# Kernel tuning notes

Hardware: AMD Instinct MI355X
Metric: run time of the kernel (lower is better)

## Reference

```python
import jax, jax.numpy as jnp
import numpy as np

SEQ, PREV, BS, D_IN, H, D = 512, 512, 8, 1024, 16, 64


def setup_inputs() -> dict:
    key = jax.random.key(0)
    ks = jax.random.split(key, 10)
    s = 0.02
    inp = {
        "input_": jax.random.normal(ks[0], (SEQ, BS, D_IN), jnp.float32),
        "pos_embs": jax.random.normal(ks[1], (SEQ + PREV, D_IN), jnp.float32),
        "memory": jax.random.normal(ks[2], (PREV, BS, D_IN), jnp.float32),
        "u": jax.random.normal(ks[3], (H, D), jnp.float32) * s,
        "v": jax.random.normal(ks[4], (H, D), jnp.float32) * s,
        # causal mask allowing full attention to memory: triu with diagonal=1+prev
        "mask": (jnp.triu(jnp.ones((SEQ, SEQ + PREV), jnp.bool_), k=1 + PREV))[..., None],
        "W_kv": jax.random.normal(ks[5], (D_IN, 2 * H * D), jnp.float32) * s,
        "W_q": jax.random.normal(ks[6], (D_IN, H * D), jnp.float32) * s,
        "W_p": jax.random.normal(ks[7], (D_IN, H * D), jnp.float32) * s,
        "W_out": jax.random.normal(ks[8], (H * D, D_IN), jnp.float32) * s,
        "ln_gamma": jnp.ones((D_IN,), jnp.float32),
        "ln_beta": jnp.zeros((D_IN,), jnp.float32),
    }
    return inp


def _rel_shift(x):
    # x: (q, k, bs, H) -> pad one zero column, reshape-transpose trick, drop first row
    q, k, bs, h = x.shape
    zp = jnp.zeros((q, 1, bs, h), x.dtype)
    return jnp.concatenate([zp, x], axis=1).reshape(k + 1, q, bs, h)[1:].reshape(q, k, bs, h)


def reference(input_, pos_embs, memory, u, v, mask, W_kv, W_q, W_p, W_out, ln_gamma, ln_beta):
    cur_seq, bs, d_in = input_.shape
    prev_seq = memory.shape[0]
    tot = cur_seq + prev_seq
    h, d = u.shape
    scale = 1.0 / d ** 0.5

    iwm = jnp.concatenate([memory, input_], axis=0)          # (tot, bs, d_in)
    kv = jnp.einsum('jbe,ef->jbf', iwm, W_kv)                 # (tot, bs, 2*H*d)
    k_t, v_t = jnp.split(kv, 2, axis=-1)
    q_t = jnp.einsum('ibe,ef->ibf', input_, W_q)              # (cur, bs, H*d)

    q4 = q_t.reshape(cur_seq, bs, h, d)
    k4 = k_t.reshape(tot, bs, h, d)
    v4 = v_t.reshape(tot, bs, h, d)

    content_attn = jnp.einsum('ibhd,jbhd->ijbh', q4 + u, k4)  # (cur, tot, bs, H)

    p_t = (pos_embs @ W_p).reshape(tot, h, d)                 # (tot, H, d)
    position_attn = jnp.einsum('ibhd,jhd->ijbh', q4 + v, p_t)
    position_attn = _rel_shift(position_attn)

    attn = content_attn + position_attn
    attn = jnp.where(mask[..., None], -jnp.inf, attn)         # mask: (cur, tot, 1) -> (cur, tot, 1, 1)
    attn = jax.nn.softmax(attn * scale, axis=1)

    awv = jnp.einsum('ijbh,jbhd->ibhd', attn, v4).reshape(cur_seq, bs, h * d)
    out = input_ + awv @ W_out                                # residual

    mu = jnp.mean(out, axis=-1, keepdims=True)
    var = jnp.mean((out - mu) ** 2, axis=-1, keepdims=True)
    out = (out - mu) / jnp.sqrt(var + 1e-5) * ln_gamma + ln_beta
    return out
```

## Files before the change

### kernel.cpp

```cpp
#include <hip/hip_runtime.h>
#include <math.h>

#define SEQ  512
#define PREV 512
#define TOT  1024
#define BSZ  8
#define DIN  1024
#define NH   16
#define HD   64

typedef __bf16 bf16;
typedef __bf16 bf16x8 __attribute__((ext_vector_type(8)));
typedef float  f32x4  __attribute__((ext_vector_type(4)));
typedef float  f32x16 __attribute__((ext_vector_type(16)));
typedef unsigned int u32;
typedef u32 u32x2 __attribute__((ext_vector_type(2)));

__device__ __forceinline__ f32x4 MFMA16(bf16x8 a, bf16x8 b, f32x4 c) {
    return __builtin_amdgcn_mfma_f32_16x16x32_bf16(a, b, c, 0, 0, 0);
}
__device__ __forceinline__ f32x16 MFMA32(bf16x8 a, bf16x8 b, f32x16 c) {
    return __builtin_amdgcn_mfma_f32_32x32x16_bf16(a, b, c, 0, 0, 0);
}

#define GLOAD16(g, l) __builtin_amdgcn_global_load_lds( \
    (const __attribute__((address_space(1))) void*)(g), \
    (__attribute__((address_space(3))) void*)(l), 16, 0, 0)

__device__ __forceinline__ unsigned short bfbits(float x) {
    return __builtin_bit_cast(unsigned short, (bf16)x);
}
__device__ __forceinline__ float bf2f(u32 bits16) {
    return __builtin_bit_cast(float, bits16 << 16);
}

__global__ __launch_bounds__(256) void cast_cat(
    const float* __restrict__ A, int nA, const float* __restrict__ B,
    bf16* __restrict__ out)
{
    int e4 = (blockIdx.x * 256 + threadIdx.x) * 4;
    float4 x = (e4 < nA) ? *(const float4*)(A + e4) : *(const float4*)(B + e4 - nA);
    union { bf16 h[4]; ushort4 u4; } pk;
    pk.h[0] = (bf16)x.x; pk.h[1] = (bf16)x.y; pk.h[2] = (bf16)x.z; pk.h[3] = (bf16)x.w;
    *(ushort4*)(out + e4) = pk.u4;
}

__global__ __launch_bounds__(256) void transcast_all(
    const float* __restrict__ W_kv, const float* __restrict__ W_q,
    const float* __restrict__ W_p,  const float* __restrict__ W_out,
    bf16* __restrict__ wkv, bf16* __restrict__ wq,
    bf16* __restrict__ wp,  bf16* __restrict__ wo)
{
    __shared__ float tile[32][33];
    const int bx = blockIdx.x;
    const float* W; bf16* Wt; int N, bn;
    if (bx < 64)       { W = W_kv;  Wt = wkv; N = 2048; bn = bx * 32; }
    else if (bx < 96)  { W = W_q;   Wt = wq;  N = 1024; bn = (bx - 64) * 32; }
    else if (bx < 128) { W = W_p;   Wt = wp;  N = 1024; bn = (bx - 96) * 32; }
    else               { W = W_out; Wt = wo;  N = 1024; bn = (bx - 128) * 32; }
    const int t = threadIdx.x;
    const int bk = blockIdx.y * 32;
    const int r = t >> 3, c4 = (t & 7) * 4;
    float4 x = *(const float4*)(W + (size_t)(bk + r) * N + bn + c4);
    tile[r][c4 + 0] = x.x; tile[r][c4 + 1] = x.y;
    tile[r][c4 + 2] = x.z; tile[r][c4 + 3] = x.w;
    __syncthreads();
    union { bf16 h[4]; ushort4 u4; } pk;
#pragma unroll
    for (int i = 0; i < 4; ++i) pk.h[i] = (bf16)tile[c4 + i][r];
    *(ushort4*)(Wt + (size_t)(bn + r) * 1024 + bk + c4) = pk.u4;
}

template<int FOUT>
__global__ __launch_bounds__(256) void gemm_mfma(
    const bf16* __restrict__ A, const bf16* __restrict__ Bt,
    const float* __restrict__ Rres, bf16* __restrict__ Cb,
    float* __restrict__ Cf, int M, int N, int K)
{
    __shared__ __align__(16) bf16 A_s[128 * 64];
    __shared__ __align__(16) bf16 B_s[128 * 64];
    const int t = threadIdx.x;
    const int w = t >> 6, lane = t & 63;
    const int li = lane & 15, hi = lane >> 4;
    const int wr = w >> 1, wc = w & 1;
    const int bm = blockIdx.y * 128, bn = blockIdx.x * 128;
    const int l3 = lane >> 3, l7 = lane & 7;
    const int srcoct = ((l7 ^ l3) * 8);

    f32x4 acc[4][4];
#pragma unroll
    for (int m = 0; m < 4; ++m)
#pragma unroll
        for (int n = 0; n < 4; ++n) acc[m][n] = (f32x4){0.f, 0.f, 0.f, 0.f};

    auto stage = [&](int k0) {
#pragma unroll
        for (int i = 0; i < 4; ++i) {
            int c = w * 4 + i;
            const bf16* ga = A + (size_t)(bm + c * 8 + l3) * K + k0 + srcoct;
            GLOAD16(ga, &A_s[c * 512]);
            const bf16* gb = Bt + (size_t)(bn + c * 8 + l3) * K + k0 + srcoct;
            GLOAD16(gb, &B_s[c * 512]);
        }
    };

    stage(0);
    const int nk = K >> 6;
    for (int ks = 0; ks < nk; ++ks) {
        __syncthreads();
#pragma unroll
        for (int kk = 0; kk < 2; ++kk) {
            bf16x8 af[4], bfr[4];
#pragma unroll
            for (int m = 0; m < 4; ++m) {
                int row = wr * 64 + m * 16 + li;
                af[m] = *(const bf16x8*)&A_s[row * 64 + ((kk * 32 + hi * 8) ^ ((row & 7) * 8))];
            }
#pragma unroll
            for (int n = 0; n < 4; ++n) {
                int row = wc * 64 + n * 16 + li;
                bfr[n] = *(const bf16x8*)&B_s[row * 64 + ((kk * 32 + hi * 8) ^ ((row & 7) * 8))];
            }
#pragma unroll
            for (int m = 0; m < 4; ++m)
#pragma unroll
                for (int n = 0; n < 4; ++n)
                    acc[m][n] = MFMA16(af[m], bfr[n], acc[m][n]);
        }
        __syncthreads();
        if (ks + 1 < nk) stage((ks + 1) << 6);
    }

#pragma unroll
    for (int m = 0; m < 4; ++m)
#pragma unroll
        for (int n = 0; n < 4; ++n)
#pragma unroll
            for (int r = 0; r < 4; ++r) {
                int row = bm + wr * 64 + m * 16 + hi * 4 + r;
                int col = bn + wc * 64 + n * 16 + li;
                size_t off = (size_t)row * N + col;
                if (FOUT) Cf[off] = acc[m][n][r] + Rres[off];
                else      Cb[off] = (bf16)acc[m][n][r];
            }
}

__global__ __launch_bounds__(256, 2) void attn_mfma(
    const bf16* __restrict__ kv, const bf16* __restrict__ qb,
    const bf16* __restrict__ pb, const float* __restrict__ u,
    const float* __restrict__ v, bf16* __restrict__ awv)
{
    const int bi = (blockIdx.z & 1) ? (3 - blockIdx.x) : blockIdx.x;
    const int i0 = bi * 128;
    const int b  = blockIdx.y;
    const int h  = blockIdx.z;
    const int t  = threadIdx.x;
    const int w  = t >> 6;
    const int lane = t & 63;
    const int ql  = lane & 31;
    const int hi2 = lane >> 5;

    __shared__ __align__(16) bf16 K_s[64 * 64];
    __shared__ __align__(16) bf16 V_s[64][72];
    __shared__ __align__(16) bf16 P_s[256 * 64];
    __shared__ __align__(16) char SCR[4][6912];

    char* rsc = SCR[w];
    char* ps  = SCR[w];

    const int c8 = t & 7;
    const int rq = t >> 3;
    const int nt = 2 * bi + 10;
    const int C0 = 384 - i0;

    bf16x8 vreg[2];
#pragma unroll
    for (int p = 0; p < 2; ++p)
        vreg[p] = *(const bf16x8*)(kv + (size_t)((p * 32 + rq) * BSZ + b) * 2048 + 1024 + h * HD + c8 * 8);
#pragma unroll
    for (int p = 0; p < 2; ++p)
        GLOAD16(kv + (size_t)((p * 32 + rq) * BSZ + b) * 2048 + h * HD + ((c8 ^ (rq & 7)) * 8),
                K_s + (p * 32 + rq) * 64 + c8 * 8);
#pragma unroll
    for (int cp = 0; cp < 6; ++cp) {
        int grow = C0 + cp * 32 + rq;
        GLOAD16(pb + (size_t)grow * DIN + h * HD + ((c8 ^ (rq & 7)) * 8),
                P_s + (grow & 255) * 64 + c8 * 8);
    }

    bf16x8 qu[4], qv[4];
    {
        const size_t qoff = ((size_t)(i0 + w * 32 + ql) * BSZ + b) * DIN + h * HD;
#pragma unroll
        for (int kk = 0; kk < 4; ++kk) {
            bf16x8 q8 = *(const bf16x8*)(qb + qoff + kk * 16 + hi2 * 8);
            const float* up = u + h * HD + kk * 16 + hi2 * 8;
            const float* vp = v + h * HD + kk * 16 + hi2 * 8;
#pragma unroll
            for (int m = 0; m < 8; ++m) {
                float qf = (float)q8[m];
                qu[kk][m] = (bf16)(qf + up[m]);
                qv[kk][m] = (bf16)(qf + vp[m]);
            }
        }
    }

    float mrun = -1e30f, lrun = 0.f;
    f32x16 o[2];
    o[0] = (f32x16){}; o[1] = (f32x16){};

    const int phq = (31 - ql) & 3;
    const int sel = phq >> 1;
    const int shb = (phq & 1) * 16;

    for (int tt = 0; tt < nt; ++tt) {
        const int j0 = tt * 64;

        __builtin_amdgcn_s_barrier();
        __builtin_amdgcn_sched_barrier(0);

#pragma unroll
        for (int p = 0; p < 2; ++p) {
            int j = p * 32 + rq;
#pragma unroll
            for (int mm = 0; mm < 8; ++mm)
                V_s[c8 * 8 + mm][(j + 8 * c8) & 63] = vreg[p][mm];
        }
        asm volatile("s_waitcnt vmcnt(0) lgkmcnt(0)" ::: "memory");
        __builtin_amdgcn_sched_barrier(0);
        __builtin_amdgcn_s_barrier();
        __builtin_amdgcn_sched_barrier(0);

        f32x16 st[2];
        st[0] = (f32x16){}; st[1] = (f32x16){};
        __builtin_amdgcn_s_setprio(1);
#pragma unroll
        for (int jt = 0; jt < 2; ++jt) {
            int row = jt * 32 + ql;
#pragma unroll
            for (int kk = 0; kk < 4; ++kk) {
                bf16x8 kf = *(const bf16x8*)&K_s[row * 64 + (((kk * 2 + hi2) ^ (ql & 7)) * 8)];
                st[jt] = MFMA32(kf, qu[kk], st[jt]);
            }
        }
        const int bwg = j0 - i0 + 480 - 32 * w;
        f32x16 rp[3];
        rp[0] = (f32x16){}; rp[1] = (f32x16){}; rp[2] = (f32x16){};
#pragma unroll
        for (int Rt = 0; Rt < 3; ++Rt) {
            int ring = (bwg + Rt * 32 + ql) & 255;
#pragma unroll
            for (int kk = 0; kk < 4; ++kk) {
                bf16x8 pf = *(const bf16x8*)&P_s[ring * 64 + (((kk * 2 + hi2) ^ (ring & 7)) * 8)];
                rp[Rt] = MFMA32(pf, qv[kk], rp[Rt]);
            }
        }
        __builtin_amdgcn_s_setprio(0);

        __builtin_amdgcn_s_barrier();
        __builtin_amdgcn_sched_barrier(0);

        if (tt + 1 < nt) {
            const int j0n = j0 + 64;
#pragma unroll
            for (int p = 0; p < 2; ++p)
                vreg[p] = *(const bf16x8*)(kv + (size_t)((j0n + p * 32 + rq) * BSZ + b) * 2048 + 1024 + h * HD + c8 * 8);
#pragma unroll
            for (int p = 0; p < 2; ++p)
                GLOAD16(kv + (size_t)((j0n + p * 32 + rq) * BSZ + b) * 2048 + h * HD + ((c8 ^ (rq & 7)) * 8),
                        K_s + (p * 32 + rq) * 64 + c8 * 8);
        }
        if (tt + 3 < nt) {
            const int Cs = C0 + (tt + 3) * 64;
#pragma unroll
            for (int p = 0; p < 2; ++p) {
                int grow = Cs + p * 32 + rq;
                GLOAD16(pb + (size_t)grow * DIN + h * HD + ((c8 ^ (rq & 7)) * 8),
                        P_s + (grow & 255) * 64 + c8 * 8);
            }
        }

#pragma unroll
        for (int Rt = 0; Rt < 3; ++Rt)
#pragma unroll
            for (int a = 0; a < 4; ++a) {
                u32 lo = (u32)bfbits(rp[Rt][a * 4 + 0]) | ((u32)bfbits(rp[Rt][a * 4 + 1]) << 16);
                u32 hi = (u32)bfbits(rp[Rt][a * 4 + 2]) | ((u32)bfbits(rp[Rt][a * 4 + 3]) << 16);
                *(u32x2*)(rsc + ql * 216 + 64 * Rt + 16 * a + 8 * hi2) = (u32x2){lo, hi};
            }

        float rowmax = -1e30f;
        const int limb = i0 + 32 * w + ql + PREV - j0;
#pragma unroll
        for (int jt = 0; jt < 2; ++jt)
#pragma unroll
            for (int a = 0; a < 4; ++a) {
                int e = jt * 32 + 8 * a + 4 * hi2 + 31 - ql;
                const u32x2* W = (const u32x2*)(rsc + ql * 216 + 8 * (e >> 2));
                u32x2 A0 = W[0], A1 = W[1];
                u32 U0 = sel ? A0[1] : A0[0];
                u32 U1 = sel ? A1[0] : A0[1];
                u32 U2 = sel ? A1[1] : A1[0];
                u32 o0 = (u32)((((unsigned long long)U1 << 32) | U0) >> shb);
                u32 o1 = (u32)((((unsigned long long)U2 << 32) | U1) >> shb);
                float pv0 = bf2f(o0 & 0xffffu), pv1 = bf2f(o0 >> 16);
                float pv2 = bf2f(o1 & 0xffffu), pv3 = bf2f(o1 >> 16);
                float pq[4] = {pv0, pv1, pv2, pv3};
#pragma unroll
                for (int rr = 0; rr < 4; ++rr) {
                    int r = a * 4 + rr;
                    int lj = jt * 32 + 8 * a + 4 * hi2 + rr;
                    float sv = (st[jt][r] + pq[rr]) * 0.125f;
                    if (lj > limb) sv = -1e30f;
                    st[jt][r] = sv;
                    rowmax = fmaxf(rowmax, sv);
                }
            }
        rowmax = fmaxf(rowmax, __shfl_xor(rowmax, 32));

        if (!__all(rowmax - mrun <= 8.f)) {
            float newm = fmaxf(mrun, rowmax);
            float fsc = __expf(mrun - newm);
#pragma unroll
            for (int r = 0; r < 16; ++r) {
                float fr = __shfl(fsc, (r & 3) + 8 * (r >> 2) + 4 * hi2);
                o[0][r] *= fr; o[1][r] *= fr;
            }
            lrun *= fsc;
            mrun = newm;
        }
        float rowsum = 0.f;
#pragma unroll
        for (int jt = 0; jt < 2; ++jt)
#pragma unroll
            for (int r = 0; r < 16; ++r) {
                float p = __expf(st[jt][r] - mrun);
                st[jt][r] = p;
                rowsum += p;
            }
        rowsum += __shfl_xor(rowsum, 32);
        lrun += rowsum;

#pragma unroll
        for (int jt = 0; jt < 2; ++jt)
#pragma unroll
            for (int a = 0; a < 4; ++a) {
                u32 lo = (u32)bfbits(st[jt][a * 4 + 0]) | ((u32)bfbits(st[jt][a * 4 + 1]) << 16);
                u32 hi = (u32)bfbits(st[jt][a * 4 + 2]) | ((u32)bfbits(st[jt][a * 4 + 3]) << 16);
                *(u32x2*)(ps + ql * 144 + 64 * jt + 16 * a + 8 * hi2) = (u32x2){lo, hi};
            }

        __builtin_amdgcn_s_setprio(1);
#pragma unroll
        for (int js = 0; js < 4; ++js) {
            bf16x8 pa = *(const bf16x8*)(ps + ql * 144 + 32 * js + 16 * hi2);
#pragma unroll
            for (int dt = 0; dt < 2; ++dt) {
                int dcol = dt * 32 + ql;
                int colb = (js * 16 + hi2 * 8 + 8 * (dcol >> 3)) & 63;
                bf16x8 vf = *(const bf16x8*)&V_s[dcol][colb];
                o[dt] = MFMA32(pa, vf, o[dt]);
            }
        }
        __builtin_amdgcn_s_setprio(0);
    }

    float lr[16];
#pragma unroll
    for (int r = 0; r < 16; ++r) lr[r] = __shfl(lrun, (r & 3) + 8 * (r >> 2) + 4 * hi2);
#pragma unroll
    for (int dt = 0; dt < 2; ++dt)
#pragma unroll
        for (int r = 0; r < 16; ++r) {
            int row = i0 + 32 * w + (r & 3) + 8 * (r >> 2) + 4 * hi2;
            awv[((size_t)row * BSZ + b) * DIN + h * HD + dt * 32 + ql] = (bf16)(o[dt][r] / lr[r]);
        }
}

__global__ __launch_bounds__(256) void ln_f32(
    float* __restrict__ out, const float* __restrict__ gamma, const float* __restrict__ beta)
{
    const int row = blockIdx.x;
    const int t = threadIdx.x;
    float4 x = *(float4*)(out + (size_t)row * DIN + t * 4);
    float s  = x.x + x.y + x.z + x.w;
    float ss = x.x * x.x + x.y * x.y + x.z * x.z + x.w * x.w;
#pragma unroll
    for (int wd = 1; wd < 64; wd <<= 1) { s += __shfl_xor(s, wd); ss += __shfl_xor(ss, wd); }
    __shared__ float sbuf[4], ssbuf[4];
    const int wave = t >> 6, lanei = t & 63;
    if (lanei == 0) { sbuf[wave] = s; ssbuf[wave] = ss; }
    __syncthreads();
    s  = sbuf[0] + sbuf[1] + sbuf[2] + sbuf[3];
    ss = ssbuf[0] + ssbuf[1] + ssbuf[2] + ssbuf[3];
    const float mu   = s * (1.f / DIN);
    const float var  = ss * (1.f / DIN) - mu * mu;
    const float rstd = rsqrtf(var + 1e-5f);
    float4 g  = *(const float4*)(gamma + t * 4);
    float4 bb = *(const float4*)(beta + t * 4);
    float4 y;
    y.x = (x.x - mu) * rstd * g.x + bb.x;
    y.y = (x.y - mu) * rstd * g.y + bb.y;
    y.z = (x.z - mu) * rstd * g.z + bb.z;
    y.w = (x.w - mu) * rstd * g.w + bb.w;
    *(float4*)(out + (size_t)row * DIN + t * 4) = y;
}

extern "C" void kernel_launch(void* const* d_in, const int* in_sizes, int n_in,
                              void* d_out, int out_size, void* d_ws, size_t ws_size,
                              hipStream_t stream)
{
    const float* input_ = (const float*)d_in[0];
    const float* pos    = (const float*)d_in[1];
    const float* memory = (const float*)d_in[2];
    const float* u      = (const float*)d_in[3];
    const float* v      = (const float*)d_in[4];
    const float* W_kv   = (const float*)d_in[6];
    const float* W_q    = (const float*)d_in[7];
    const float* W_p    = (const float*)d_in[8];
    const float* W_out  = (const float*)d_in[9];
    const float* gamma  = (const float*)d_in[10];
    const float* beta   = (const float*)d_in[11];

    bf16* iwm  = (bf16*)d_ws;
    bf16* kvb  = iwm  + (size_t)8192 * 1024;
    bf16* qbf  = kvb  + (size_t)8192 * 2048;
    bf16* pbf  = qbf  + (size_t)4096 * 1024;
    bf16* posb = pbf  + (size_t)1024 * 1024;
    bf16* wkv  = posb + (size_t)1024 * 1024;
    bf16* wq   = wkv  + (size_t)2048 * 1024;
    bf16* wp   = wq   + (size_t)1024 * 1024;
    bf16* wo   = wp   + (size_t)1024 * 1024;
    bf16* awvb = wo   + (size_t)1024 * 1024;
    float* outf = (float*)d_out;

    cast_cat<<<8192, 256, 0, stream>>>(memory, 4194304, input_, iwm);
    cast_cat<<<1024, 256, 0, stream>>>(pos, 1048576, pos, posb);
    transcast_all<<<dim3(160, 32), 256, 0, stream>>>(W_kv, W_q, W_p, W_out, wkv, wq, wp, wo);

    gemm_mfma<0><<<dim3(16, 64), 256, 0, stream>>>(iwm, wkv, nullptr, kvb, nullptr, 8192, 2048, 1024);
    gemm_mfma<0><<<dim3(8, 32), 256, 0, stream>>>(iwm + (size_t)4096 * 1024, wq, nullptr, qbf, nullptr, 4096, 1024, 1024);
    gemm_mfma<0><<<dim3(8, 8),  256, 0, stream>>>(posb, wp, nullptr, pbf, nullptr, 1024, 1024, 1024);

    attn_mfma<<<dim3(4, 8, 16), 256, 0, stream>>>(kvb, qbf, pbf, u, v, awvb);

    gemm_mfma<1><<<dim3(8, 32), 256, 0, stream>>>(awvb, wo, input_, nullptr, outf, 4096, 1024, 1024);
    ln_f32<<<4096, 256, 0, stream>>>(outf, gamma, beta);
}
```

Measured before the change: 205.3 us.

## Add 256x256 phased GEMM for KV projection, fuse cast kernels, use exp2 softmax

Replaces the KV projection GEMM with a new 512-thread kernel that uses 256x256 tiles and double-buffered LDS. It splits each K-step into four phases, interleaving staging loads and MFMA batches with explicit waitcnt and barriers, and remaps blocks so each XCD gets a group of neighbouring M tiles. The two cast kernels become one launch. The attention softmax folds log2(e) into the scale and uses exp2, with the rescale threshold raised to match. The aim is more data reuse and overlap in the largest GEMM and less launch and exp overhead, at the cost of one block per CU and high register pressure.

```diff
diff --git a/kernel.cpp b/kernel.cpp
--- a/kernel.cpp
+++ b/kernel.cpp
@@ -34,15 +34,24 @@
     return __builtin_bit_cast(float, bits16 << 16);
 }
 
-__global__ __launch_bounds__(256) void cast_cat(
-    const float* __restrict__ A, int nA, const float* __restrict__ B,
-    bf16* __restrict__ out)
-{
-    int e4 = (blockIdx.x * 256 + threadIdx.x) * 4;
-    float4 x = (e4 < nA) ? *(const float4*)(A + e4) : *(const float4*)(B + e4 - nA);
+__global__ __launch_bounds__(256) void cast_all(
+    const float* __restrict__ memory, const float* __restrict__ input_,
+    const float* __restrict__ pos, bf16* __restrict__ iwm, bf16* __restrict__ posb)
+{
+    const int bid = blockIdx.x;
+    const float* src; bf16* dst; int e4;
+    if (bid < 8192) {
+        e4 = (bid * 256 + threadIdx.x) * 4;
+        src = (e4 < 4194304) ? memory : input_ - 4194304;
+        dst = iwm;
+    } else {
+        e4 = ((bid - 8192) * 256 + threadIdx.x) * 4;
+        src = pos; dst = posb;
+    }
+    float4 x = *(const float4*)(src + e4);
     union { bf16 h[4]; ushort4 u4; } pk;
     pk.h[0] = (bf16)x.x; pk.h[1] = (bf16)x.y; pk.h[2] = (bf16)x.z; pk.h[3] = (bf16)x.w;
-    *(ushort4*)(out + e4) = pk.u4;
+    *(ushort4*)(dst + e4) = pk.u4;
 }
 
 __global__ __launch_bounds__(256) void transcast_all(
@@ -71,6 +80,106 @@
     *(ushort4*)(Wt + (size_t)(bn + r) * 1024 + bk + c4) = pk.u4;
 }
 
+__global__ __launch_bounds__(512, 1) void gemm_8ph(
+    const bf16* __restrict__ A, const bf16* __restrict__ Bt,
+    bf16* __restrict__ C, int M, int N, int K)
+{
+    __shared__ __align__(16) bf16 A_s[2][256 * 64];
+    __shared__ __align__(16) bf16 B_s[2][256 * 64];
+    const int t = threadIdx.x;
+    const int w = t >> 6, lane = t & 63;
+    const int li = lane & 15, hi = lane >> 4;
+    const int wm = w >> 2, wn = w & 3;
+    const int lin = blockIdx.y * 8 + blockIdx.x;
+    const int xcd = lin & 7, idx = lin >> 3;
+    const int bm = (xcd * 4 + (idx & 3)) * 256;
+    const int bn = (idx >> 2) * 256;
+
+    f32x4 acc[8][4];
+#pragma unroll
+    for (int m = 0; m < 8; ++m)
+#pragma unroll
+        for (int n = 0; n < 4; ++n) acc[m][n] = (f32x4){0.f, 0.f, 0.f, 0.f};
+
+    auto stage_half = [&](int buf, int ks, int h) {
+        const bf16* __restrict__ src = (h < 2) ? A : Bt;
+        const int base = (h < 2) ? bm : bn;
+        const int hh = (h & 1) * 128;
+        bf16* dst = (h < 2) ? &A_s[buf][0] : &B_s[buf][0];
+        const int k0 = ks << 6;
+#pragma unroll
+        for (int g = 0; g < 2; ++g) {
+            const int row = hh + g * 64 + (t >> 3);
+            const bf16* gp = src + (size_t)(base + row) * K + k0 + (((t & 7) ^ (row & 7)) * 8);
+            GLOAD16(gp, dst + (size_t)(hh + g * 64 + w * 8) * 64);
+        }
+    };
+
+    bf16x8 af[4], bfr[4];
+    auto LDA = [&](int buf, int mh, int kk) {
+#pragma unroll
+        for (int m = 0; m < 4; ++m) {
+            int row = wm * 128 + (mh * 4 + m) * 16 + li;
+            af[m] = *(const bf16x8*)&A_s[buf][row * 64 + (((kk * 4 + hi) ^ (row & 7)) * 8)];
+        }
+    };
+    auto LDB = [&](int buf, int kk) {
+#pragma unroll
+        for (int n = 0; n < 4; ++n) {
+            int row = wn * 64 + n * 16 + li;
+            bfr[n] = *(const bf16x8*)&B_s[buf][row * 64 + (((kk * 4 + hi) ^ (row & 7)) * 8)];
+        }
+    };
+
+#define FMA_PHASE(mh)                                                    \
+    asm volatile("s_waitcnt lgkmcnt(0)" ::: "memory");                   \
+    __builtin_amdgcn_sched_barrier(0);                                   \
+    __builtin_amdgcn_s_setprio(1);                                       \
+    _Pragma("unroll")                                                    \
+    for (int m = 0; m < 4; ++m)                                          \
+        _Pragma("unroll")                                                \
+        for (int n = 0; n < 4; ++n)                                      \
+            acc[(mh) * 4 + m][n] = MFMA16(af[m], bfr[n], acc[(mh) * 4 + m][n]); \
+    __builtin_amdgcn_s_setprio(0);                                       \
+    __builtin_amdgcn_s_barrier();
+
+    stage_half(0, 0, 0); stage_half(0, 0, 1); stage_half(0, 0, 2); stage_half(0, 0, 3);
+
+    const int nk = K >> 6;
+    for (int ks = 0; ks < nk; ++ks) {
+        const int cur = ks & 1, nxt = cur ^ 1;
+        const int ksn = (ks + 1 < nk) ? ks + 1 : ks;
+        stage_half(nxt, ksn, 0);
+        asm volatile("s_waitcnt vmcnt(2)" ::: "memory");
+        __builtin_amdgcn_sched_barrier(0);
+        __builtin_amdgcn_s_barrier();
+        LDB(cur, 0); LDA(cur, 0, 0);
+        FMA_PHASE(0)
+        stage_half(nxt, ksn, 1);
+        LDA(cur, 1, 0);
+        FMA_PHASE(1)
+        stage_half(nxt, ksn, 2);
+        LDB(cur, 1); LDA(cur, 0, 1);
+        FMA_PHASE(0)
+        stage_half(nxt, ksn, 3);
+        LDA(cur, 1, 1);
+        FMA_PHASE(1)
+    }
+    asm volatile("s_waitcnt vmcnt(0)" ::: "memory");
+
+#pragma unroll
+    for (int m = 0; m < 8; ++m)
+#pragma unroll
+        for (int n = 0; n < 4; ++n)
+#pragma unroll
+            for (int r = 0; r < 4; ++r) {
+                int row = bm + wm * 128 + m * 16 + hi * 4 + r;
+                int col = bn + wn * 64 + n * 16 + li;
+                C[(size_t)row * N + col] = (bf16)acc[m][n][r];
+            }
+#undef FMA_PHASE
+}
+
 template<int FOUT>
 __global__ __launch_bounds__(256) void gemm_mfma(
     const bf16* __restrict__ A, const bf16* __restrict__ Bt,
@@ -172,6 +281,7 @@
     const int rq = t >> 3;
     const int nt = 2 * bi + 10;
     const int C0 = 384 - i0;
+    const float SCL = 0.125f * 1.44269504088896f;
 
     bf16x8 vreg[2];
 #pragma unroll
@@ -303,14 +413,13 @@
                 u32 U2 = sel ? A1[1] : A1[0];
                 u32 o0 = (u32)((((unsigned long long)U1 << 32) | U0) >> shb);
                 u32 o1 = (u32)((((unsigned long long)U2 << 32) | U1) >> shb);
-                float pv0 = bf2f(o0 & 0xffffu), pv1 = bf2f(o0 >> 16);
-                float pv2 = bf2f(o1 & 0xffffu), pv3 = bf2f(o1 >> 16);
-                float pq[4] = {pv0, pv1, pv2, pv3};
+                float pq[4] = {bf2f(o0 & 0xffffu), bf2f(o0 >> 16),
+                               bf2f(o1 & 0xffffu), bf2f(o1 >> 16)};
 #pragma unroll
                 for (int rr = 0; rr < 4; ++rr) {
                     int r = a * 4 + rr;
                     int lj = jt * 32 + 8 * a + 4 * hi2 + rr;
-                    float sv = (st[jt][r] + pq[rr]) * 0.125f;
+                    float sv = (st[jt][r] + pq[rr]) * SCL;
                     if (lj > limb) sv = -1e30f;
                     st[jt][r] = sv;
                     rowmax = fmaxf(rowmax, sv);
@@ -318,9 +427,9 @@
             }
         rowmax = fmaxf(rowmax, __shfl_xor(rowmax, 32));
 
-        if (!__all(rowmax - mrun <= 8.f)) {
+        if (!__all(rowmax - mrun <= 11.5f)) {
             float newm = fmaxf(mrun, rowmax);
-            float fsc = __expf(mrun - newm);
+            float fsc = exp2f(mrun - newm);
 #pragma unroll
             for (int r = 0; r < 16; ++r) {
                 float fr = __shfl(fsc, (r & 3) + 8 * (r >> 2) + 4 * hi2);
@@ -334,7 +443,7 @@
         for (int jt = 0; jt < 2; ++jt)
 #pragma unroll
             for (int r = 0; r < 16; ++r) {
-                float p = __expf(st[jt][r] - mrun);
+                float p = exp2f(st[jt][r] - mrun);
                 st[jt][r] = p;
                 rowsum += p;
             }
@@ -434,11 +543,10 @@
     bf16* awvb = wo   + (size_t)1024 * 1024;
     float* outf = (float*)d_out;
 
-    cast_cat<<<8192, 256, 0, stream>>>(memory, 4194304, input_, iwm);
-    cast_cat<<<1024, 256, 0, stream>>>(pos, 1048576, pos, posb);
+    cast_all<<<9216, 256, 0, stream>>>(memory, input_, pos, iwm, posb);
     transcast_all<<<dim3(160, 32), 256, 0, stream>>>(W_kv, W_q, W_p, W_out, wkv, wq, wp, wo);
 
-    gemm_mfma<0><<<dim3(16, 64), 256, 0, stream>>>(iwm, wkv, nullptr, kvb, nullptr, 8192, 2048, 1024);
+    gemm_8ph<<<dim3(8, 32), 512, 0, stream>>>(iwm, wkv, kvb, 8192, 2048, 1024);
     gemm_mfma<0><<<dim3(8, 32), 256, 0, stream>>>(iwm + (size_t)4096 * 1024, wq, nullptr, qbf, nullptr, 4096, 1024, 1024);
     gemm_mfma<0><<<dim3(8, 8),  256, 0, stream>>>(posb, wp, nullptr, pbf, nullptr, 1024, 1024, 1024);
 
```

Result: slower. 211.8 us (+3.1%).
